# Kernel tuning notes

Hardware: AMD Instinct MI355X
Metric: run time of the kernel (lower is better)

## Reference

```python
import jax, jax.numpy as jnp
import numpy as np

B, S, H = 2, 2048, 4096
NQ, NKV, D = 32, 8, 128
EPS = 1e-6
THETA = 1000000.0


def rms_norm(x, w, eps=EPS):
    # normalize over last dim (per-head RMSNorm on head_dim)
    var = jnp.mean(jnp.square(x), axis=-1, keepdims=True)
    return x * jax.lax.rsqrt(var + eps) * w


def rope(x, positions, theta=THETA):
    # x: [B, S, N, D]; rotate-half convention (Qwen/Llama style)
    d = x.shape[-1]
    inv_freq = 1.0 / (theta ** (jnp.arange(0, d, 2, dtype=jnp.float32) / d))  # [D/2]
    ang = positions[:, None].astype(jnp.float32) * inv_freq[None, :]          # [S, D/2]
    cos = jnp.cos(ang)[None, :, None, :]
    sin = jnp.sin(ang)[None, :, None, :]
    x1, x2 = x[..., : d // 2], x[..., d // 2 :]
    return jnp.concatenate([x1 * cos - x2 * sin, x2 * cos + x1 * sin], axis=-1)


def setup_inputs() -> dict:
    key = jax.random.key(0)
    ks = jax.random.split(key, 7)
    sc_in = 1.0 / np.sqrt(H)
    sc_out = 1.0 / np.sqrt(NQ * D)
    return {
        "x": jax.random.normal(ks[0], (B, S, H), jnp.float32),
        "wq": jax.random.normal(ks[1], (H, NQ * D), jnp.float32) * sc_in,
        "wk": jax.random.normal(ks[2], (H, NKV * D), jnp.float32) * sc_in,
        "wv": jax.random.normal(ks[3], (H, NKV * D), jnp.float32) * sc_in,
        "wo": jax.random.normal(ks[4], (NQ * D, H), jnp.float32) * sc_out,
        "q_norm_w": jnp.ones((D,), jnp.float32),
        "k_norm_w": jnp.ones((D,), jnp.float32),
    }


def reference(x, wq, wk, wv, wo, q_norm_w, k_norm_w):
    b, s, _ = x.shape
    positions = jnp.arange(s)

    q = (x @ wq).reshape(b, s, NQ, D)   # [B,S,NQ,D]
    k = (x @ wk).reshape(b, s, NKV, D)  # [B,S,NKV,D]
    v = (x @ wv).reshape(b, s, NKV, D)

    # per-head QK RMSNorm, then RoPE
    q = rope(rms_norm(q, q_norm_w), positions)
    k = rope(rms_norm(k, k_norm_w), positions)

    # GQA: expand kv heads to query heads (group = NQ // NKV)
    g = NQ // NKV
    k = jnp.repeat(k, g, axis=2)  # [B,S,NQ,D]
    v = jnp.repeat(v, g, axis=2)

    scale = D ** -0.5
    scores = jnp.einsum("bqhd,bkhd->bhqk", q, k) * scale  # [B,NQ,S,S]
    causal = jnp.tril(jnp.ones((s, s), bool))
    scores = jnp.where(causal[None, None], scores, jnp.finfo(scores.dtype).min)
    attn = jax.nn.softmax(scores, axis=-1)

    out = jnp.einsum("bhqk,bkhd->bqhd", attn, v).reshape(b, s, NQ * D)
    return out @ wo
```

## Files before the change

### kernel.cpp

```cpp
#include <hip/hip_runtime.h>
#include <hip/hip_bf16.h>

#define DEV __device__ __forceinline__

typedef unsigned short u16;
typedef unsigned int u32;
typedef __attribute__((ext_vector_type(8))) short short8;
typedef __attribute__((ext_vector_type(4))) float f32x4;
typedef __attribute__((ext_vector_type(16))) float f32x16;

static constexpr int Bb = 2, Ss = 2048, Hh = 4096, NQ = 32, NKV = 8, Dd = 128;
static constexpr int Mm = Bb * Ss;

DEV u16 f2bf(float f) {
    u32 u = __float_as_uint(f);
    u32 r = (u + 0x7fffu + ((u >> 16) & 1u)) >> 16;
    return (u16)r;
}
DEV float bf2f(u16 b) { return __uint_as_float((u32)b << 16); }
DEV u32 cvtpk(float lo, float hi) {
    u32 r;
    asm("v_cvt_pk_bf16_f32 %0, %1, %2" : "=v"(r) : "v"(lo), "v"(hi));
    return r;
}

__global__ void k_cast(const float4* __restrict__ in, ushort4* __restrict__ out, int n4) {
    int i = blockIdx.x * 256 + threadIdx.x;
    if (i < n4) {
        float4 v = in[i];
        ushort4 o;
        o.x = f2bf(v.x); o.y = f2bf(v.y); o.z = f2bf(v.z); o.w = f2bf(v.w);
        out[i] = o;
    }
}

__global__ __launch_bounds__(256) void k_transpose(const float* __restrict__ in, u16* __restrict__ out,
                                                   int R, int C) {
    __shared__ u16 t[64][68];
    int tx = threadIdx.x & 15, ty = threadIdx.x >> 4;
    long tr = (long)blockIdx.y * 64, tc = (long)blockIdx.x * 64;
    #pragma unroll
    for (int j = 0; j < 4; j++) {
        int r = ty + j * 16;
        float4 v = *(const float4*)&in[(tr + r) * C + tc + tx * 4];
        t[tx * 4 + 0][r] = f2bf(v.x);
        t[tx * 4 + 1][r] = f2bf(v.y);
        t[tx * 4 + 2][r] = f2bf(v.z);
        t[tx * 4 + 3][r] = f2bf(v.w);
    }
    __syncthreads();
    #pragma unroll
    for (int j = 0; j < 4; j++) {
        int c = ty + j * 16;
        *(ushort4*)&out[(tc + c) * R + tr + tx * 4] = *(ushort4*)&t[c][tx * 4];
    }
}

DEV void gld16(const void* g, void* l) {
    __builtin_amdgcn_global_load_lds((const __attribute__((address_space(1))) void*)g,
                                     (__attribute__((address_space(3))) void*)l, 16, 0, 0);
}

#define FENCE asm volatile("" ::: "memory")

template <int MODE>
__global__ __launch_bounds__(512) void k_gemm256(const u16* __restrict__ A, const u16* __restrict__ B0,
                                                 void* __restrict__ C0, void* __restrict__ C1,
                                                 void* __restrict__ C2, int M, int N, int K, int nbx) {
    constexpr int NF = (MODE == 3) ? 3 : 4;
    __shared__ u16 S[2][16384 + NF * 4096];
    const int tid = threadIdx.x, lane = tid & 63, wid = tid >> 6;
    const int wr = wid >> 2, wc = wid & 3;
    const int l = blockIdx.x;
    const int bx = l % nbx, by = l / nbx;
    const long m0 = (long)by * 256, n0 = (long)bx * (NF * 64);
    const int r15 = lane & 15;
    const int cch0 = 8 * ((lane >> 4) ^ (r15 & 7));

    const u16 *pA[4], *pB[NF];
    {
        int rl = lane >> 3;
        int sc = 8 * ((lane & 7) ^ rl);
        #pragma unroll
        for (int j = 0; j < 4; j++)
            pA[j] = A + (m0 + (wid * 4 + j) * 8 + rl) * (long)K + sc;
        #pragma unroll
        for (int j = 0; j < NF; j++)
            pB[j] = B0 + (n0 + (wid * NF + j) * 8 + rl) * (long)K + sc;
    }

    f32x4 acc[8][NF];
    #pragma unroll
    for (int i = 0; i < 8; i++)
        #pragma unroll
        for (int j = 0; j < NF; j++) acc[i][j] = f32x4{0.f, 0.f, 0.f, 0.f};

    const int NT = K / 64;
    auto STAGE = [&](int t) {
        int tb = t & 1; long ko = (long)t * 64;
        #pragma unroll
        for (int j = 0; j < NF; j++) gld16(pB[j] + ko, (void*)&S[tb][16384 + (wid * NF + j) * 512]);
        #pragma unroll
        for (int j = 0; j < 4; j++) gld16(pA[j] + ko, (void*)&S[tb][(wid * 4 + j) * 512]);
    };

    const int aro = wr * 8192 + r15 * 64 + cch0;
    const int bro = 16384 + wc * (NF * 1024) + r15 * 64 + cch0;

    STAGE(0);
    asm volatile("s_waitcnt vmcnt(0)" ::: "memory");
    FENCE; __builtin_amdgcn_s_barrier(); FENCE;

    short8 af[4][2], bf[NF][2];
    for (int kt = 0; kt < NT; ++kt) {
        const u16* Sb = S[kt & 1];
        if (kt + 1 < NT) STAGE(kt + 1);
        #pragma unroll
        for (int n = 0; n < NF; n++) {
            bf[n][0] = *(const short8*)&Sb[bro + n * 1024];
            bf[n][1] = *(const short8*)&Sb[(bro + n * 1024) ^ 32];
        }
        #pragma unroll
        for (int m = 0; m < 4; m++) {
            af[m][0] = *(const short8*)&Sb[aro + m * 1024];
            af[m][1] = *(const short8*)&Sb[(aro + m * 1024) ^ 32];
        }
        __builtin_amdgcn_s_setprio(1);
        #pragma unroll
        for (int m = 0; m < 4; m++)
            #pragma unroll
            for (int n = 0; n < NF; n++) {
                acc[m][n] = __builtin_amdgcn_mfma_f32_16x16x32_bf16(af[m][0], bf[n][0], acc[m][n], 0, 0, 0);
                acc[m][n] = __builtin_amdgcn_mfma_f32_16x16x32_bf16(af[m][1], bf[n][1], acc[m][n], 0, 0, 0);
            }
        __builtin_amdgcn_s_setprio(0);
        short8 ag[4][2];
        #pragma unroll
        for (int m = 0; m < 4; m++) {
            ag[m][0] = *(const short8*)&Sb[aro + (m + 4) * 1024];
            ag[m][1] = *(const short8*)&Sb[(aro + (m + 4) * 1024) ^ 32];
        }
        __builtin_amdgcn_s_setprio(1);
        #pragma unroll
        for (int m = 0; m < 4; m++)
            #pragma unroll
            for (int n = 0; n < NF; n++) {
                acc[m + 4][n] = __builtin_amdgcn_mfma_f32_16x16x32_bf16(ag[m][0], bf[n][0], acc[m + 4][n], 0, 0, 0);
                acc[m + 4][n] = __builtin_amdgcn_mfma_f32_16x16x32_bf16(ag[m][1], bf[n][1], acc[m + 4][n], 0, 0, 0);
            }
        __builtin_amdgcn_s_setprio(0);
        if (kt + 1 < NT) asm volatile("s_waitcnt vmcnt(0)" ::: "memory");
        FENCE; __builtin_amdgcn_s_barrier(); FENCE;
    }

    const int rq = (lane >> 4) * 4;
    #pragma unroll
    for (int m = 0; m < 8; m++) {
        #pragma unroll
        for (int n = 0; n < NF; n++) {
            long row0 = m0 + wr * 128 + m * 16 + rq;
            long col = n0 + wc * (NF * 16) + n * 16 + r15;
            if (MODE == 0) {
                float* Cf = (float*)C0;
                #pragma unroll
                for (int i = 0; i < 4; i++) Cf[(row0 + i) * N + col] = acc[m][n][i];
            } else {
                if (col < 4096) {
                    u16* Cb = (u16*)C0;
                    #pragma unroll
                    for (int i = 0; i < 4; i++) Cb[(row0 + i) * 4096 + col] = f2bf(acc[m][n][i]);
                } else if (col < 5120) {
                    u16* Cb = (u16*)C1;
                    long cl = col - 4096;
                    #pragma unroll
                    for (int i = 0; i < 4; i++) Cb[(row0 + i) * 1024 + cl] = f2bf(acc[m][n][i]);
                } else {
                    u16* Cb = (u16*)C2;
                    long cl = col - 5120;
                    ushort4 pk;
                    pk.x = f2bf(acc[m][n][0]);
                    pk.y = f2bf(acc[m][n][1]);
                    pk.z = f2bf(acc[m][n][2]);
                    pk.w = f2bf(acc[m][n][3]);
                    *(ushort4*)&Cb[cl * Mm + row0] = pk;
                }
            }
        }
    }
}

__global__ __launch_bounds__(256) void k_normrope(u16* __restrict__ buf,
                                                  const float* __restrict__ w, int NH, float oscale) {
    int row = blockIdx.x * 4 + (threadIdx.x >> 6);
    int lane = threadIdx.x & 63;
    long base = (long)row * 128;
    float x1 = bf2f(buf[base + lane]), x2 = bf2f(buf[base + lane + 64]);
    float ss = x1 * x1 + x2 * x2;
    #pragma unroll
    for (int m = 1; m < 64; m <<= 1) ss += __shfl_xor(ss, m);
    float r = rsqrtf(ss * (1.f / 128.f) + 1e-6f);
    float n1 = x1 * r * w[lane], n2 = x2 * r * w[lane + 64];
    int pos = (row / NH) % Ss;
    float invf = exp2f((float)lane * (-19.931568569324174f / 64.f));
    float ang = (float)pos * invf;
    float c = cosf(ang), sn = sinf(ang);
    buf[base + lane] = f2bf((n1 * c - n2 * sn) * oscale);
    buf[base + lane + 64] = f2bf((n2 * c + n1 * sn) * oscale);
}

__global__ __launch_bounds__(256, 2) void k_attn(const u16* __restrict__ Q, const u16* __restrict__ Kb,
                                                 const u16* __restrict__ Vg, u16* __restrict__ O) {
    __shared__ u16 KT[2][64 * 128];
    __shared__ u16 VT[2][128 * 64];
    int tid = threadIdx.x, lane = tid & 63, wid = tid >> 6;
    int d0 = blockIdx.x;
    int L = (d0 & 7) * 64 + (d0 >> 3);
    int pr = L & 31;
    int hk = (L >> 5) & 7;
    int b = L >> 8;
    int h = hk * 4 + wid;
    int q0a = pr * 32;
    int q0b = (63 - pr) * 32;
    int c31 = lane & 31, hi5 = lane >> 5;
    int kx16 = (c31 & 15) << 3;
    int kx8 = (c31 & 7) << 3;

    short8 qfa[8], qfb[8];
    {
        const u16* qra = Q + ((long)(b * Ss + q0a + c31) * NQ + h) * Dd + hi5 * 8;
        const u16* qrb = Q + ((long)(b * Ss + q0b + c31) * NQ + h) * Dd + hi5 * 8;
        #pragma unroll
        for (int c = 0; c < 8; c++) {
            qfa[c] = *(const short8*)(qra + c * 16);
            qfb[c] = *(const short8*)(qrb + c * 16);
        }
    }

    const u16* kg[4];
    const u16* vg[4];
    int i0 = wid * 4;
    #pragma unroll
    for (int ii = 0; ii < 4; ii++) {
        int i = i0 + ii;
        int r = i * 4 + (lane >> 4);
        kg[ii] = Kb + ((long)(b * Ss + r) * NKV + hk) * Dd + 8 * ((lane & 15) ^ (r & 15));
        int d = i * 8 + (lane >> 3);
        vg[ii] = Vg + (long)(hk * Dd + d) * Mm + (long)b * Ss + 8 * ((lane & 7) ^ (d & 7));
    }

    f32x16 oaa[4], oab[4];
    #pragma unroll
    for (int f = 0; f < 4; f++)
        #pragma unroll
        for (int r = 0; r < 16; r++) { oaa[f][r] = 0.f; oab[f][r] = 0.f; }
    float mra = -INFINITY, lra = 0.f, mrb = -INFINITY, lrb = 0.f;

    const long kadv = (long)64 * NKV * Dd;
    int nt = q0b / 64 + 1;
    int cur = 0;

    auto STEP = [&](int k0, int q0, const short8 (&qf)[8], f32x16 (&oa)[4],
                    float& mrun, float& lrun) {
        int ql = q0 + c31;
        int krow = k0 & 32;
        f32x16 st;
        #pragma unroll
        for (int r = 0; r < 16; r++) st[r] = 0.f;
        __builtin_amdgcn_s_setprio(1);
        #pragma unroll
        for (int c = 0; c < 8; c++) {
            short8 kf = *(const short8*)&KT[cur][(krow + c31) * 128 + ((c * 16 + hi5 * 8) ^ kx16)];
            st = __builtin_amdgcn_mfma_f32_32x32x16_bf16(kf, qf[c], st, 0, 0, 0);
        }
        __builtin_amdgcn_s_setprio(0);
        float p[16];
        if (k0 + 31 > q0) {
            #pragma unroll
            for (int r = 0; r < 16; r++) {
                int kidx = k0 + (r & 3) + 8 * (r >> 2) + 4 * hi5;
                p[r] = (kidx > ql) ? -INFINITY : st[r];
            }
        } else {
            #pragma unroll
            for (int r = 0; r < 16; r++) p[r] = st[r];
        }
        float pmax = p[0];
        #pragma unroll
        for (int r = 1; r < 16; r++) pmax = fmaxf(pmax, p[r]);
        pmax = fmaxf(pmax, __shfl_xor(pmax, 32));
        if (!__all(pmax - mrun <= 8.f)) {
            float mnew = fmaxf(mrun, pmax);
            float sc = __builtin_amdgcn_exp2f(mrun - mnew);
            lrun *= sc;
            #pragma unroll
            for (int f = 0; f < 4; f++)
                #pragma unroll
                for (int r = 0; r < 16; r++) oa[f][r] *= sc;
            mrun = mnew;
        }
        float ls = 0.f;
        #pragma unroll
        for (int r = 0; r < 16; r++) {
            float e = __builtin_amdgcn_exp2f(p[r] - mrun);
            p[r] = e;
            ls += e;
        }
        ls += __shfl_xor(ls, 32);
        lrun += ls;

        u32 w0 = cvtpk(p[0], p[1]), w1 = cvtpk(p[2], p[3]);
        u32 w2 = cvtpk(p[4], p[5]), w3 = cvtpk(p[6], p[7]);
        u32 w4 = cvtpk(p[8], p[9]), w5 = cvtpk(p[10], p[11]);
        u32 w6 = cvtpk(p[12], p[13]), w7 = cvtpk(p[14], p[15]);
        u32 x0 = (u32)__shfl_xor((int)w0, 32), x1 = (u32)__shfl_xor((int)w1, 32);
        u32 x2 = (u32)__shfl_xor((int)w2, 32), x3 = (u32)__shfl_xor((int)w3, 32);
        u32 x4 = (u32)__shfl_xor((int)w4, 32), x5 = (u32)__shfl_xor((int)w5, 32);
        u32 x6 = (u32)__shfl_xor((int)w6, 32), x7 = (u32)__shfl_xor((int)w7, 32);
        union { u32 u[4]; short8 s; } pb0, pb1;
        if (hi5) {
            pb0.u[0] = x2; pb0.u[1] = x3; pb0.u[2] = w2; pb0.u[3] = w3;
            pb1.u[0] = x6; pb1.u[1] = x7; pb1.u[2] = w6; pb1.u[3] = w7;
        } else {
            pb0.u[0] = w0; pb0.u[1] = w1; pb0.u[2] = x0; pb0.u[3] = x1;
            pb1.u[0] = w4; pb1.u[1] = w5; pb1.u[2] = x4; pb1.u[3] = x5;
        }
        __builtin_amdgcn_s_setprio(1);
        #pragma unroll
        for (int f = 0; f < 4; f++) {
            int d = 32 * f + c31;
            const u16* vrow = &VT[cur][d * 64];
            short8 v0 = *(const short8*)&vrow[(krow + hi5 * 8) ^ kx8];
            short8 v1 = *(const short8*)&vrow[(krow + 16 + hi5 * 8) ^ kx8];
            oa[f] = __builtin_amdgcn_mfma_f32_32x32x16_bf16(v0, pb0.s, oa[f], 0, 0, 0);
            oa[f] = __builtin_amdgcn_mfma_f32_32x32x16_bf16(v1, pb1.s, oa[f], 0, 0, 0);
        }
        __builtin_amdgcn_s_setprio(0);
    };

    #pragma unroll
    for (int ii = 0; ii < 4; ii++) {
        gld16(kg[ii], &KT[0][(i0 + ii) * 512]);
        gld16(vg[ii], &VT[0][(i0 + ii) * 512]);
    }
    __syncthreads();

    for (int t = 0; t < nt; ++t) {
        if (t + 1 < nt) {
            long ko = (long)(t + 1) * kadv;
            int vo = (t + 1) * 64;
            #pragma unroll
            for (int ii = 0; ii < 4; ii++) {
                gld16(kg[ii] + ko, &KT[cur ^ 1][(i0 + ii) * 512]);
                gld16(vg[ii] + vo, &VT[cur ^ 1][(i0 + ii) * 512]);
            }
        }
        #pragma unroll
        for (int ks = 0; ks < 2; ++ks) {
            int k0 = t * 64 + ks * 32;
            if (k0 <= q0a + 31) STEP(k0, q0a, qfa, oaa, mra, lra);
            if (k0 <= q0b + 31) STEP(k0, q0b, qfb, oab, mrb, lrb);
        }
        __syncthreads();
        cur ^= 1;
    }

    #pragma unroll
    for (int x = 0; x < 2; x++) {
        int q0 = x ? q0b : q0a;
        f32x16* oa = x ? oab : oaa;
        float linv = 1.f / (x ? lrb : lra);
        u16* orow = O + ((long)(b * Ss + q0 + c31) * NQ + h) * Dd;
        #pragma unroll
        for (int f = 0; f < 4; f++) {
            #pragma unroll
            for (int rq = 0; rq < 4; rq++) {
                int dbase = 32 * f + 8 * rq + 4 * hi5;
                union { u32 u[2]; ushort4 v; } pk;
                pk.u[0] = cvtpk(oa[f][4 * rq + 0] * linv, oa[f][4 * rq + 1] * linv);
                pk.u[1] = cvtpk(oa[f][4 * rq + 2] * linv, oa[f][4 * rq + 3] * linv);
                *(ushort4*)(orow + dbase) = pk.v;
            }
        }
    }
}

extern "C" void kernel_launch(void* const* d_in, const int* in_sizes, int n_in,
                              void* d_out, int out_size, void* d_ws, size_t ws_size,
                              hipStream_t stream) {
    (void)in_sizes; (void)n_in; (void)out_size; (void)ws_size;
    const float* x = (const float*)d_in[0];
    const float* wq = (const float*)d_in[1];
    const float* wk = (const float*)d_in[2];
    const float* wv = (const float*)d_in[3];
    const float* wo = (const float*)d_in[4];
    const float* qnw = (const float*)d_in[5];
    const float* knw = (const float*)d_in[6];

    char* ws = (char*)d_ws;
    const size_t MB = 1024 * 1024;
    const float qscale = (float)(0.08838834764831845 * 1.4426950408889634);

    u16* xb = (u16*)(ws);
    u16* Wqkv = (u16*)(ws + 32 * MB);
    u16* qb = (u16*)(ws + 80 * MB);
    u16* kb = (u16*)(ws + 112 * MB);
    u16* vt = (u16*)(ws + 120 * MB);
    u16* ao = xb;
    u16* WoT = Wqkv;

    int n4 = Mm * Hh / 4;
    k_cast<<<n4 / 256, 256, 0, stream>>>((const float4*)x, (ushort4*)xb, n4);

    k_transpose<<<dim3(Hh / 64, Hh / 64), 256, 0, stream>>>(wq, Wqkv, Hh, Hh);
    k_transpose<<<dim3((NKV * Dd) / 64, Hh / 64), 256, 0, stream>>>(wk, Wqkv + (size_t)4096 * Hh, Hh, NKV * Dd);
    k_transpose<<<dim3((NKV * Dd) / 64, Hh / 64), 256, 0, stream>>>(wv, Wqkv + (size_t)5120 * Hh, Hh, NKV * Dd);

    k_gemm256<3><<<32 * (Mm / 256), 512, 0, stream>>>(xb, Wqkv, qb, kb, vt, Mm, 6144, Hh, 32);

    k_normrope<<<(Mm * NQ) / 4, 256, 0, stream>>>(qb, qnw, NQ, qscale);
    k_normrope<<<(Mm * NKV) / 4, 256, 0, stream>>>(kb, knw, NKV, 1.0f);

    k_attn<<<512, 256, 0, stream>>>(qb, kb, vt, ao);

    k_transpose<<<dim3(Hh / 64, Hh / 64), 256, 0, stream>>>(wo, WoT, Hh, Hh);
    k_gemm256<0><<<16 * (Mm / 256), 512, 0, stream>>>(ao, WoT, d_out, nullptr, nullptr, Mm, Hh, NQ * Dd, 16);
}
```

Measured before the change: 524.7 us.

## Fuse Q RMSNorm and RoPE into attention prologue; reorder GEMM MFMA chains

Removes the separate Q norm+RoPE kernel. Each attention wave now normalizes and rotates its Q fragments in registers right after loading them, which avoids writing and re-reading the full Q tensor. In exchange, the normalization and rotation work is repeated per block with sincos in registers, adding register pressure. Separately, the GEMM inner loop is split into two passes over the k-halves so consecutive MFMAs target different accumulators, reducing dependent-issue stalls.

```diff
diff --git a/kernel.cpp b/kernel.cpp
--- a/kernel.cpp
+++ b/kernel.cpp
@@ -129,10 +129,13 @@
         #pragma unroll
         for (int m = 0; m < 4; m++)
             #pragma unroll
-            for (int n = 0; n < NF; n++) {
+            for (int n = 0; n < NF; n++)
                 acc[m][n] = __builtin_amdgcn_mfma_f32_16x16x32_bf16(af[m][0], bf[n][0], acc[m][n], 0, 0, 0);
+        #pragma unroll
+        for (int m = 0; m < 4; m++)
+            #pragma unroll
+            for (int n = 0; n < NF; n++)
                 acc[m][n] = __builtin_amdgcn_mfma_f32_16x16x32_bf16(af[m][1], bf[n][1], acc[m][n], 0, 0, 0);
-            }
         __builtin_amdgcn_s_setprio(0);
         short8 ag[4][2];
         #pragma unroll
@@ -144,10 +147,13 @@
         #pragma unroll
         for (int m = 0; m < 4; m++)
             #pragma unroll
-            for (int n = 0; n < NF; n++) {
+            for (int n = 0; n < NF; n++)
                 acc[m + 4][n] = __builtin_amdgcn_mfma_f32_16x16x32_bf16(ag[m][0], bf[n][0], acc[m + 4][n], 0, 0, 0);
+        #pragma unroll
+        for (int m = 0; m < 4; m++)
+            #pragma unroll
+            for (int n = 0; n < NF; n++)
                 acc[m + 4][n] = __builtin_amdgcn_mfma_f32_16x16x32_bf16(ag[m][1], bf[n][1], acc[m + 4][n], 0, 0, 0);
-            }
         __builtin_amdgcn_s_setprio(0);
         if (kt + 1 < NT) asm volatile("s_waitcnt vmcnt(0)" ::: "memory");
         FENCE; __builtin_amdgcn_s_barrier(); FENCE;
@@ -209,7 +215,8 @@
 }
 
 __global__ __launch_bounds__(256, 2) void k_attn(const u16* __restrict__ Q, const u16* __restrict__ Kb,
-                                                 const u16* __restrict__ Vg, u16* __restrict__ O) {
+                                                 const u16* __restrict__ Vg, u16* __restrict__ O,
+                                                 const float* __restrict__ qw, float qscale) {
     __shared__ u16 KT[2][64 * 128];
     __shared__ u16 VT[2][128 * 64];
     int tid = threadIdx.x, lane = tid & 63, wid = tid >> 6;
@@ -235,6 +242,34 @@
             qfb[c] = *(const short8*)(qrb + c * 16);
         }
     }
+    auto NORMQ = [&](short8 (&qf)[8], int q0) {
+        float ss = 0.f;
+        #pragma unroll
+        for (int c = 0; c < 8; c++)
+            #pragma unroll
+            for (int j = 0; j < 8; j++) {
+                float x = bf2f(((const u16*)&qf[c])[j]);
+                ss += x * x;
+            }
+        ss += __shfl_xor(ss, 32);
+        float rn = rsqrtf(ss * (1.f / 128.f) + 1e-6f);
+        float pos = (float)(q0 + c31);
+        #pragma unroll
+        for (int c = 0; c < 4; c++) {
+            #pragma unroll
+            for (int j = 0; j < 8; j++) {
+                int d64 = c * 16 + hi5 * 8 + j;
+                float x1 = bf2f(((const u16*)&qf[c])[j]) * rn * qw[d64];
+                float x2 = bf2f(((const u16*)&qf[c + 4])[j]) * rn * qw[d64 + 64];
+                float ang = pos * exp2f((float)d64 * (-19.931568569324174f / 64.f));
+                float cs = cosf(ang), sn = sinf(ang);
+                ((u16*)&qf[c])[j]     = f2bf((x1 * cs - x2 * sn) * qscale);
+                ((u16*)&qf[c + 4])[j] = f2bf((x2 * cs + x1 * sn) * qscale);
+            }
+        }
+    };
+    NORMQ(qfa, q0a);
+    NORMQ(qfb, q0b);
 
     const u16* kg[4];
     const u16* vg[4];
@@ -417,10 +452,9 @@
 
     k_gemm256<3><<<32 * (Mm / 256), 512, 0, stream>>>(xb, Wqkv, qb, kb, vt, Mm, 6144, Hh, 32);
 
-    k_normrope<<<(Mm * NQ) / 4, 256, 0, stream>>>(qb, qnw, NQ, qscale);
     k_normrope<<<(Mm * NKV) / 4, 256, 0, stream>>>(kb, knw, NKV, 1.0f);
 
-    k_attn<<<512, 256, 0, stream>>>(qb, kb, vt, ao);
+    k_attn<<<512, 256, 0, stream>>>(qb, kb, vt, ao, qnw, qscale);
 
     k_transpose<<<dim3(Hh / 64, Hh / 64), 256, 0, stream>>>(wo, WoT, Hh, Hh);
     k_gemm256<0><<<16 * (Mm / 256), 512, 0, stream>>>(ao, WoT, d_out, nullptr, nullptr, Mm, Hh, NQ * Dd, 16);
```

New measurement: 690.5 us. 31.6% more time.
